# Optimization experiments

Measured on AMD Instinct MI355X. Metric: run time of the kernel, lower is better.

Reference implementation:

```python
import jax, jax.numpy as jnp
import numpy as np

D_MODEL = 1024
N_HEAD = 16
B, S = 4, 1024


def _linear(x, W, b):
    # torch nn.Linear: y = x @ W.T + b, W: [out, in]
    return jnp.einsum('bsd,ed->bse', x, W) + b


def _split(x):
    b, s, d = x.shape
    return x.reshape(b, s, N_HEAD, d // N_HEAD).transpose(0, 2, 1, 3)  # [b,h,s,dh]


def _concat(x):
    b, h, s, dh = x.shape
    return x.transpose(0, 2, 1, 3).reshape(b, s, h * dh)


def _attention(q, k, v):
    dh = q.shape[-1]
    scale = 1.0 / np.float32(np.sqrt(dh))
    scores = jnp.einsum('bhqd,bhkd->bhqk', q, k) * scale
    probs = jax.nn.softmax(scores, axis=-1)
    return jnp.einsum('bhqk,bhkd->bhqd', probs, v)


def setup_inputs() -> dict:
    key = jax.random.key(0)
    ks = jax.random.split(key, 20)
    sc = 1.0 / np.float32(np.sqrt(D_MODEL))
    inp = {
        'q': jax.random.normal(ks[0], (B, S, D_MODEL), jnp.float32),
        'k': jax.random.normal(ks[1], (B, S, D_MODEL), jnp.float32),
        'v': jax.random.normal(ks[2], (B, S, D_MODEL), jnp.float32),
    }
    names = ['Wq', 'Wk', 'Wv', 'Wq2', 'Wk2', 'Wv2', 'Wc', 'Wc2']
    for i, n in enumerate(names):
        inp[n] = jax.random.normal(ks[3 + i], (D_MODEL, D_MODEL), jnp.float32) * sc
        inp['b' + n[1:]] = jnp.zeros((D_MODEL,), jnp.float32)
    return inp


def reference(q, k, v, Wq, bq, Wk, bk, Wv, bv, Wq2, bq2, Wk2, bk2, Wv2, bv2, Wc, bc, Wc2, bc2):
    # path 1 projections
    q1 = _linear(q, Wq, bq)
    k1 = _linear(k, Wk, bk)
    v1 = _linear(v, Wv, bv)
    # path 2 projections (note cross-wiring: q2 from k, k2/v2 from q)
    q2 = _linear(k, Wq2, bq2)
    k2 = _linear(q, Wk2, bk2)
    v2 = _linear(q, Wv2, bv2)

    out1 = _attention(_split(q1), _split(k1), _split(v1))
    out2 = _attention(_split(q2), _split(k2), _split(v2))

    out1 = _linear(_concat(out1), Wc, bc)
    out2 = _linear(_concat(out2), Wc2, bc2)
    return out1, out2
```

## Files before the change

### kernel.cpp

```cpp
#include <hip/hip_runtime.h>
#include <hip/hip_bf16.h>

#define B_ 4
#define S_ 1024
#define D_ 1024
#define H_ 16
#define M_ 4096

typedef unsigned short u16;
typedef __attribute__((ext_vector_type(4))) float f32x4;
typedef __attribute__((ext_vector_type(16))) float f32x16;
typedef __attribute__((ext_vector_type(8))) short short8;
typedef __attribute__((ext_vector_type(4))) u16 u16x4;

__device__ inline u16 f2bf(float f) {
  return __builtin_bit_cast(u16, __float2bfloat16(f));
}

__device__ inline short8 ldfrag(const u16* p) {
  return *reinterpret_cast<const short8*>(p);
}

__device__ inline void gload_lds16(const void* g, void* l) {
  __builtin_amdgcn_global_load_lds((const __attribute__((address_space(1))) void*)g,
                                   (__attribute__((address_space(3))) void*)l,
                                   16, 0, 0);
}

__device__ inline int sigma_s(int s) {
  return (s & ~12) | ((s & 4) << 1) | ((s & 8) >> 1);
}

struct GArgs {
  const void* A[6];
  const void* W[6];
  const float* bias[6];
  void* C[6];
  float oscale[6];
  int vtrans[6];
};

struct CvtArgs {
  const float* src[11];
  u16* dst[11];
  int n4[11];
};

__global__ __launch_bounds__(256) void cvt_f32_bf16(CvtArgs a) {
  const int z = blockIdx.y;
  const float4* s = (const float4*)a.src[z];
  u16x4* d = (u16x4*)a.dst[z];
  const int n4 = a.n4[z];
  for (int i = blockIdx.x * blockDim.x + threadIdx.x; i < n4; i += gridDim.x * blockDim.x) {
    float4 v = s[i];
    u16x4 o;
    o[0] = f2bf(v.x); o[1] = f2bf(v.y); o[2] = f2bf(v.z); o[3] = f2bf(v.w);
    d[i] = o;
  }
}

template<typename CT>
__global__ __launch_bounds__(512, 1) void gemm_ring(GArgs args) {
  const int z = blockIdx.z;
  const u16* A = (const u16*)args.A[z];
  const u16* W = (const u16*)args.W[z];
  const float* bias = args.bias[z];
  CT* C = (CT*)args.C[z];
  const float oscale = args.oscale[z];
  const int vtrans = args.vtrans[z];

  __shared__ u16 LA[3][256 * 64];
  __shared__ u16 LB[3][128 * 64];

  const int tid = threadIdx.x;
  const int lane = tid & 63;
  const int w = tid >> 6;
  const int wm = w >> 1, wn = w & 1;
  const int l15 = lane & 15, lhi = lane >> 4;

  const int nwg = gridDim.x * gridDim.y;
  const int lin = blockIdx.x + blockIdx.y * gridDim.x;
  const int swz = (lin & 7) * (nwg >> 3) + (lin >> 3);
  const int bx = swz % gridDim.x, by = swz / gridDim.x;
  const int m0 = by * 256, n0 = bx * 128;

  const int srow = tid >> 3;
  const int sgcol = (((tid & 7) ^ (srow & 7)) << 3);

  f32x4 acc[4][4];
#pragma unroll
  for (int m = 0; m < 4; ++m)
#pragma unroll
    for (int n = 0; n < 4; ++n) acc[m][n] = f32x4{0.f, 0.f, 0.f, 0.f};

  const u16* Abase = A + (size_t)m0 * 1024;
  const u16* Wbase = W + (size_t)n0 * 1024;

  auto stage = [&](int ktile, int r) {
    const u16* Ag = Abase + ktile * 64;
    const u16* Wg = Wbase + ktile * 64;
#pragma unroll
    for (int i = 0; i < 4; ++i)
      gload_lds16(Ag + (size_t)(i * 64 + srow) * 1024 + sgcol, &LA[r][i * 4096 + w * 512]);
#pragma unroll
    for (int i = 0; i < 2; ++i)
      gload_lds16(Wg + (size_t)(i * 64 + srow) * 1024 + sgcol, &LB[r][i * 4096 + w * 512]);
  };

  stage(0, 0);
  stage(1, 1);
  asm volatile("s_waitcnt vmcnt(6)" ::: "memory");
  __builtin_amdgcn_s_barrier();
  __builtin_amdgcn_sched_barrier(0);

  for (int t = 0; t < 16; ++t) {
    const int kp = (t + 2 < 16) ? t + 2 : 15;
    stage(kp, (t + 2) % 3);

    const int r = t % 3;
#pragma unroll
    for (int kk = 0; kk < 2; ++kk) {
      short8 af[4], bf[4];
#pragma unroll
      for (int m = 0; m < 4; ++m) {
        int row = wm * 64 + m * 16 + l15;
        af[m] = ldfrag(&LA[r][row * 64 + (((kk * 4 + lhi) ^ (row & 7)) << 3)]);
      }
#pragma unroll
      for (int n = 0; n < 4; ++n) {
        int row = wn * 64 + n * 16 + l15;
        bf[n] = ldfrag(&LB[r][row * 64 + (((kk * 4 + lhi) ^ (row & 7)) << 3)]);
      }
      __builtin_amdgcn_s_setprio(1);
#pragma unroll
      for (int m = 0; m < 4; ++m)
#pragma unroll
        for (int n = 0; n < 4; ++n)
          acc[m][n] = __builtin_amdgcn_mfma_f32_16x16x32_bf16(af[m], bf[n], acc[m][n], 0, 0, 0);
      __builtin_amdgcn_s_setprio(0);
    }

    asm volatile("s_waitcnt vmcnt(6)" ::: "memory");
    __builtin_amdgcn_s_barrier();
    __builtin_amdgcn_sched_barrier(0);
  }

#pragma unroll
  for (int m = 0; m < 4; ++m) {
#pragma unroll
    for (int n = 0; n < 4; ++n) {
      int ncol = n0 + wn * 64 + n * 16 + l15;
      float bsv = bias[ncol];
      int mb = m0 + wm * 64 + m * 16 + lhi * 4;
      if (vtrans) {
        int h = ncol >> 6, d = ncol & 63;
        int b = mb >> 10, s0 = sigma_s(mb & 1023);
        u16x4 ov;
#pragma unroll
        for (int r2 = 0; r2 < 4; ++r2) ov[r2] = f2bf((acc[m][n][r2] + bsv) * oscale);
        *reinterpret_cast<u16x4*>((u16*)C + ((size_t)((b * 16 + h) * 64 + d)) * 1024 + s0) = ov;
      } else {
#pragma unroll
        for (int r2 = 0; r2 < 4; ++r2) {
          float val = (acc[m][n][r2] + bsv) * oscale;
          if constexpr (sizeof(CT) == 2) ((u16*)C)[(size_t)(mb + r2) * 1024 + ncol] = f2bf(val);
          else ((float*)C)[(size_t)(mb + r2) * 1024 + ncol] = val;
        }
      }
    }
  }
}

template<typename AT, typename CT>
__global__ __launch_bounds__(256) void gemm_bt_batched(GArgs args) {
  const int z = blockIdx.z;
  const AT* A = (const AT*)args.A[z];
  const float* W = (const float*)args.W[z];
  const float* bias = args.bias[z];
  CT* C = (CT*)args.C[z];
  const float oscale = args.oscale[z];
  const int vtrans = args.vtrans[z];

  __shared__ u16 Al[128][72];
  __shared__ u16 Bl[128][72];

  const int tid = threadIdx.x;
  const int lane = tid & 63;
  const int wid = tid >> 6;
  const int wr = wid >> 1, wc = wid & 1;
  const int m0 = blockIdx.y * 128, n0 = blockIdx.x * 128;
  const int l15 = lane & 15, lhi = lane >> 4;

  const f32x4 vzero = {0.f, 0.f, 0.f, 0.f};
  f32x4 acc[4][4];
#pragma unroll
  for (int i = 0; i < 4; ++i)
#pragma unroll
    for (int j = 0; j < 4; ++j) acc[i][j] = vzero;

  for (int kt = 0; kt < 1024; kt += 64) {
    __syncthreads();
#pragma unroll
    for (int i = 0; i < 8; ++i) {
      int g = tid + i * 256;
      int row = g >> 4, col = (g & 15) * 4;
      u16x4 bv;
      if constexpr (sizeof(AT) == 4) {
        float4 vv = *reinterpret_cast<const float4*>((const float*)A + (size_t)(m0 + row) * 1024 + kt + col);
        bv[0] = f2bf(vv.x); bv[1] = f2bf(vv.y); bv[2] = f2bf(vv.z); bv[3] = f2bf(vv.w);
      } else {
        bv = *reinterpret_cast<const u16x4*>((const u16*)A + (size_t)(m0 + row) * 1024 + kt + col);
      }
      *reinterpret_cast<u16x4*>(&Al[row][col]) = bv;
    }
#pragma unroll
    for (int i = 0; i < 8; ++i) {
      int g = tid + i * 256;
      int row = g >> 4, col = (g & 15) * 4;
      float4 vv = *reinterpret_cast<const float4*>((const float*)W + (size_t)(n0 + row) * 1024 + kt + col);
      u16x4 bv;
      bv[0] = f2bf(vv.x); bv[1] = f2bf(vv.y); bv[2] = f2bf(vv.z); bv[3] = f2bf(vv.w);
      *reinterpret_cast<u16x4*>(&Bl[row][col]) = bv;
    }
    __syncthreads();

#pragma unroll
    for (int c = 0; c < 2; ++c) {
      short8 af[4], bfr[4];
#pragma unroll
      for (int i = 0; i < 4; ++i) af[i] = ldfrag(&Al[wr * 64 + i * 16 + l15][c * 32 + lhi * 8]);
#pragma unroll
      for (int j = 0; j < 4; ++j) bfr[j] = ldfrag(&Bl[wc * 64 + j * 16 + l15][c * 32 + lhi * 8]);
#pragma unroll
      for (int i = 0; i < 4; ++i)
#pragma unroll
        for (int j = 0; j < 4; ++j)
          acc[i][j] = __builtin_amdgcn_mfma_f32_16x16x32_bf16(af[i], bfr[j], acc[i][j], 0, 0, 0);
    }
  }

#pragma unroll
  for (int i = 0; i < 4; ++i) {
#pragma unroll
    for (int j = 0; j < 4; ++j) {
      int n = n0 + wc * 64 + j * 16 + l15;
      float bsv = bias[n];
      int mb = m0 + wr * 64 + i * 16 + lhi * 4;
      if (vtrans) {
        int h = n >> 6, d = n & 63;
        int b = mb >> 10, s0 = sigma_s(mb & 1023);
        u16x4 ov;
#pragma unroll
        for (int r = 0; r < 4; ++r) ov[r] = f2bf((acc[i][j][r] + bsv) * oscale);
        *reinterpret_cast<u16x4*>((u16*)C + ((size_t)((b * 16 + h) * 64 + d)) * 1024 + s0) = ov;
      } else {
#pragma unroll
        for (int r = 0; r < 4; ++r) {
          float val = (acc[i][j][r] + bsv) * oscale;
          if constexpr (sizeof(CT) == 2) ((u16*)C)[(size_t)(mb + r) * 1024 + n] = f2bf(val);
          else ((float*)C)[(size_t)(mb + r) * 1024 + n] = val;
        }
      }
    }
  }
}

__global__ __launch_bounds__(256, 2) void attn_fused32b(const u16* q1b, const u16* k1b, const u16* vt1,
                                                        const u16* q2b, const u16* k2b, const u16* vt2,
                                                        u16* o1, u16* o2) {
  const int qt = blockIdx.x;
  const int h = blockIdx.y;
  const int zb = blockIdx.z;
  const int path = zb >> 2, b = zb & 3;

  const u16* Q = (path == 0) ? q1b : q2b;
  const u16* K = (path == 0) ? k1b : k2b;
  const u16* V = (path == 0) ? vt1 : vt2;
  u16* O = (path == 0) ? o1 : o2;

  const size_t base_qk = (size_t)b * S_ * D_ + (size_t)h * 64;
  const size_t vbase = (size_t)((b * 16 + h) * 64) * 1024;
  const int tid = threadIdx.x;
  const int lane = tid & 63, w = tid >> 6;
  const int lq = lane & 31, hi = lane >> 5;

  __shared__ u16 Ks[2][64][72];
  __shared__ u16 Vs[2][64][72];

  const int srow = tid >> 3;
  const int scol = (tid & 7) * 8;

  const int qbase_row = qt * 256 + w * 64;
  short8 qf[2][4];
#pragma unroll
  for (int qtile = 0; qtile < 2; ++qtile)
#pragma unroll
    for (int dhg = 0; dhg < 4; ++dhg)
      qf[qtile][dhg] = ldfrag(Q + base_qk + (size_t)(qbase_row + qtile * 32 + lq) * 1024 + dhg * 16 + hi * 8);

  f32x16 o_acc[2][2] = {};
  float m_r[2] = {-1e30f, -1e30f};
  float l_r[2] = {0.f, 0.f};

  {
    short8 r0 = ldfrag(K + base_qk + (size_t)srow * 1024 + scol);
    short8 r1 = ldfrag(K + base_qk + (size_t)(srow + 32) * 1024 + scol);
    short8 r2 = ldfrag(V + vbase + (size_t)srow * 1024 + scol);
    short8 r3 = ldfrag(V + vbase + (size_t)(srow + 32) * 1024 + scol);
    *reinterpret_cast<short8*>(&Ks[0][srow][scol]) = r0;
    *reinterpret_cast<short8*>(&Ks[0][srow + 32][scol]) = r1;
    *reinterpret_cast<short8*>(&Vs[0][srow][scol]) = r2;
    *reinterpret_cast<short8*>(&Vs[0][srow + 32][scol]) = r3;
  }
  __syncthreads();

  for (int kv = 0; kv < 16; ++kv) {
    const int cur = kv & 1;

    short8 n0, n1, n2, n3;
    if (kv < 15) {
      const u16* kg = K + base_qk + (size_t)((kv + 1) * 64) * 1024;
      const u16* vg = V + vbase + (kv + 1) * 64;
      n0 = ldfrag(kg + (size_t)srow * 1024 + scol);
      n1 = ldfrag(kg + (size_t)(srow + 32) * 1024 + scol);
      n2 = ldfrag(vg + (size_t)srow * 1024 + scol);
      n3 = ldfrag(vg + (size_t)(srow + 32) * 1024 + scol);
    }

    f32x16 s[2][2] = {};
    __builtin_amdgcn_s_setprio(1);
#pragma unroll
    for (int dhg = 0; dhg < 4; ++dhg) {
#pragma unroll
      for (int keytile = 0; keytile < 2; ++keytile) {
        short8 ka = ldfrag(&Ks[cur][keytile * 32 + lq][dhg * 16 + hi * 8]);
#pragma unroll
        for (int qtile = 0; qtile < 2; ++qtile)
          s[keytile][qtile] = __builtin_amdgcn_mfma_f32_32x32x16_bf16(ka, qf[qtile][dhg], s[keytile][qtile], 0, 0, 0);
      }
    }
    __builtin_amdgcn_s_setprio(0);

#pragma unroll
    for (int qtile = 0; qtile < 2; ++qtile) {
      float pm = s[0][qtile][0];
#pragma unroll
      for (int r = 1; r < 16; ++r) pm = fmaxf(pm, s[0][qtile][r]);
#pragma unroll
      for (int r = 0; r < 16; ++r) pm = fmaxf(pm, s[1][qtile][r]);
      pm = fmaxf(pm, __shfl_xor(pm, 32));
      float mn = fmaxf(m_r[qtile], pm);
      float sc = __expf(m_r[qtile] - mn);
      m_r[qtile] = mn;
      float sum = 0.f;
#pragma unroll
      for (int kt = 0; kt < 2; ++kt)
#pragma unroll
        for (int r = 0; r < 16; ++r) {
          float e = __expf(s[kt][qtile][r] - mn);
          s[kt][qtile][r] = e;
          sum += e;
        }
      sum += __shfl_xor(sum, 32);
      l_r[qtile] = l_r[qtile] * sc + sum;
      o_acc[0][qtile] *= sc;
      o_acc[1][qtile] *= sc;
    }

    __builtin_amdgcn_s_setprio(1);
#pragma unroll
    for (int g = 0; g < 4; ++g) {
      short8 va0 = ldfrag(&Vs[cur][lq][g * 16 + hi * 8]);
      short8 va1 = ldfrag(&Vs[cur][32 + lq][g * 16 + hi * 8]);
#pragma unroll
      for (int qtile = 0; qtile < 2; ++qtile) {
        short8 pb;
#pragma unroll
        for (int j = 0; j < 8; ++j) {
          float pv = (g < 2) ? s[0][qtile][(g & 1) * 8 + j] : s[1][qtile][(g & 1) * 8 + j];
          pb[j] = (short)f2bf(pv);
        }
        o_acc[0][qtile] = __builtin_amdgcn_mfma_f32_32x32x16_bf16(va0, pb, o_acc[0][qtile], 0, 0, 0);
        o_acc[1][qtile] = __builtin_amdgcn_mfma_f32_32x32x16_bf16(va1, pb, o_acc[1][qtile], 0, 0, 0);
      }
    }
    __builtin_amdgcn_s_setprio(0);

    __syncthreads();
    if (kv < 15) {
      const int nxt = cur ^ 1;
      *reinterpret_cast<short8*>(&Ks[nxt][srow][scol]) = n0;
      *reinterpret_cast<short8*>(&Ks[nxt][srow + 32][scol]) = n1;
      *reinterpret_cast<short8*>(&Vs[nxt][srow][scol]) = n2;
      *reinterpret_cast<short8*>(&Vs[nxt][srow + 32][scol]) = n3;
      __syncthreads();
    }
  }

#pragma unroll
  for (int qtile = 0; qtile < 2; ++qtile) {
    float inv = 1.0f / l_r[qtile];
    u16* Op = O + base_qk + (size_t)(qbase_row + qtile * 32 + lq) * 1024;
#pragma unroll
    for (int dtile = 0; dtile < 2; ++dtile) {
#pragma unroll
      for (int qd = 0; qd < 4; ++qd) {
        u16x4 ov;
#pragma unroll
        for (int r = 0; r < 4; ++r) ov[r] = f2bf(o_acc[dtile][qtile][qd * 4 + r] * inv);
        *reinterpret_cast<u16x4*>(Op + dtile * 32 + 8 * qd + 4 * hi) = ov;
      }
    }
  }
}

extern "C" void kernel_launch(void* const* d_in, const int* in_sizes, int n_in,
                              void* d_out, int out_size, void* d_ws, size_t ws_size,
                              hipStream_t stream) {
  const float* q   = (const float*)d_in[0];
  const float* k   = (const float*)d_in[1];
  const float* v   = (const float*)d_in[2];
  const float* Wq  = (const float*)d_in[3];  const float* bq  = (const float*)d_in[4];
  const float* Wk  = (const float*)d_in[5];  const float* bk  = (const float*)d_in[6];
  const float* Wv  = (const float*)d_in[7];  const float* bv  = (const float*)d_in[8];
  const float* Wq2 = (const float*)d_in[9];  const float* bq2 = (const float*)d_in[10];
  const float* Wk2 = (const float*)d_in[11]; const float* bk2 = (const float*)d_in[12];
  const float* Wv2 = (const float*)d_in[13]; const float* bv2 = (const float*)d_in[14];
  const float* Wc  = (const float*)d_in[15]; const float* bc  = (const float*)d_in[16];
  const float* Wc2 = (const float*)d_in[17]; const float* bc2 = (const float*)d_in[18];

  u16* ws = (u16*)d_ws;
  const size_t SZ = (size_t)M_ * D_;
  const size_t WSZ = (size_t)D_ * D_;
  u16* q1b = ws + 0 * SZ;
  u16* k1b = ws + 1 * SZ;
  u16* vt1 = ws + 2 * SZ;
  u16* q2b = ws + 3 * SZ;
  u16* k2b = ws + 4 * SZ;
  u16* vt2 = ws + 5 * SZ;
  u16* a1  = ws + 6 * SZ;
  u16* a2  = ws + 7 * SZ;

  const size_t need = (11 * SZ + 8 * WSZ) * sizeof(u16);

  if (ws_size >= need) {
    u16* qb = ws + 8 * SZ;
    u16* kb = ws + 9 * SZ;
    u16* vb = ws + 10 * SZ;
    u16* wbase = ws + 11 * SZ;
    u16* WqB  = wbase + 0 * WSZ;
    u16* WkB  = wbase + 1 * WSZ;
    u16* WvB  = wbase + 2 * WSZ;
    u16* Wq2B = wbase + 3 * WSZ;
    u16* Wk2B = wbase + 4 * WSZ;
    u16* Wv2B = wbase + 5 * WSZ;
    u16* WcB  = wbase + 6 * WSZ;
    u16* Wc2B = wbase + 7 * WSZ;

    CvtArgs ca;
    ca.src[0] = q;   ca.dst[0] = qb;   ca.n4[0] = (int)(SZ / 4);
    ca.src[1] = k;   ca.dst[1] = kb;   ca.n4[1] = (int)(SZ / 4);
    ca.src[2] = v;   ca.dst[2] = vb;   ca.n4[2] = (int)(SZ / 4);
    ca.src[3] = Wq;  ca.dst[3] = WqB;  ca.n4[3] = (int)(WSZ / 4);
    ca.src[4] = Wk;  ca.dst[4] = WkB;  ca.n4[4] = (int)(WSZ / 4);
    ca.src[5] = Wv;  ca.dst[5] = WvB;  ca.n4[5] = (int)(WSZ / 4);
    ca.src[6] = Wq2; ca.dst[6] = Wq2B; ca.n4[6] = (int)(WSZ / 4);
    ca.src[7] = Wk2; ca.dst[7] = Wk2B; ca.n4[7] = (int)(WSZ / 4);
    ca.src[8] = Wv2; ca.dst[8] = Wv2B; ca.n4[8] = (int)(WSZ / 4);
    ca.src[9] = Wc;  ca.dst[9] = WcB;  ca.n4[9] = (int)(WSZ / 4);
    ca.src[10] = Wc2; ca.dst[10] = Wc2B; ca.n4[10] = (int)(WSZ / 4);
    cvt_f32_bf16<<<dim3(512, 11), dim3(256), 0, stream>>>(ca);

    GArgs pa;
    pa.A[0] = qb; pa.W[0] = WqB;  pa.bias[0] = bq;  pa.C[0] = q1b; pa.oscale[0] = 0.125f; pa.vtrans[0] = 0;
    pa.A[1] = kb; pa.W[1] = WkB;  pa.bias[1] = bk;  pa.C[1] = k1b; pa.oscale[1] = 1.0f;   pa.vtrans[1] = 0;
    pa.A[2] = vb; pa.W[2] = WvB;  pa.bias[2] = bv;  pa.C[2] = vt1; pa.oscale[2] = 1.0f;   pa.vtrans[2] = 1;
    pa.A[3] = kb; pa.W[3] = Wq2B; pa.bias[3] = bq2; pa.C[3] = q2b; pa.oscale[3] = 0.125f; pa.vtrans[3] = 0;
    pa.A[4] = qb; pa.W[4] = Wk2B; pa.bias[4] = bk2; pa.C[4] = k2b; pa.oscale[4] = 1.0f;   pa.vtrans[4] = 0;
    pa.A[5] = qb; pa.W[5] = Wv2B; pa.bias[5] = bv2; pa.C[5] = vt2; pa.oscale[5] = 1.0f;   pa.vtrans[5] = 1;
    gemm_ring<u16><<<dim3(8, 16, 6), dim3(512), 0, stream>>>(pa);

    attn_fused32b<<<dim3(4, 16, 8), dim3(256), 0, stream>>>(q1b, k1b, vt1, q2b, k2b, vt2, a1, a2);

    GArgs fa;
    fa.A[0] = a1; fa.W[0] = WcB;  fa.bias[0] = bc;  fa.C[0] = (float*)d_out;      fa.oscale[0] = 1.0f; fa.vtrans[0] = 0;
    fa.A[1] = a2; fa.W[1] = Wc2B; fa.bias[1] = bc2; fa.C[1] = (float*)d_out + SZ; fa.oscale[1] = 1.0f; fa.vtrans[1] = 0;
    gemm_ring<float><<<dim3(8, 16, 2), dim3(512), 0, stream>>>(fa);
  } else {
    GArgs pa;
    pa.A[0] = q; pa.W[0] = Wq;  pa.bias[0] = bq;  pa.C[0] = q1b; pa.oscale[0] = 0.125f; pa.vtrans[0] = 0;
    pa.A[1] = k; pa.W[1] = Wk;  pa.bias[1] = bk;  pa.C[1] = k1b; pa.oscale[1] = 1.0f;   pa.vtrans[1] = 0;
    pa.A[2] = v; pa.W[2] = Wv;  pa.bias[2] = bv;  pa.C[2] = vt1; pa.oscale[2] = 1.0f;   pa.vtrans[2] = 1;
    pa.A[3] = k; pa.W[3] = Wq2; pa.bias[3] = bq2; pa.C[3] = q2b; pa.oscale[3] = 0.125f; pa.vtrans[3] = 0;
    pa.A[4] = q; pa.W[4] = Wk2; pa.bias[4] = bk2; pa.C[4] = k2b; pa.oscale[4] = 1.0f;   pa.vtrans[4] = 0;
    pa.A[5] = q; pa.W[5] = Wv2; pa.bias[5] = bv2; pa.C[5] = vt2; pa.oscale[5] = 1.0f;   pa.vtrans[5] = 1;
    gemm_bt_batched<float, u16><<<dim3(8, 32, 6), dim3(256), 0, stream>>>(pa);

    attn_fused32b<<<dim3(4, 16, 8), dim3(256), 0, stream>>>(q1b, k1b, vt1, q2b, k2b, vt2, a1, a2);

    GArgs fa;
    fa.A[0] = a1; fa.W[0] = Wc;  fa.bias[0] = bc;  fa.C[0] = (float*)d_out;      fa.oscale[0] = 1.0f; fa.vtrans[0] = 0;
    fa.A[1] = a2; fa.W[1] = Wc2; fa.bias[1] = bc2; fa.C[1] = (float*)d_out + SZ; fa.oscale[1] = 1.0f; fa.vtrans[1] = 0;
    gemm_bt_batched<u16, float><<<dim3(8, 32, 2), dim3(256), 0, stream>>>(fa);
  }
}
```

Baseline: 180.4 us.

## Split projection GEMM K-step into two phases interleaving global loads with MFMA

```diff
diff --git a/kernel.cpp b/kernel.cpp
--- a/kernel.cpp
+++ b/kernel.cpp
@@ -96,49 +96,84 @@
   const u16* Abase = A + (size_t)m0 * 1024;
   const u16* Wbase = W + (size_t)n0 * 1024;
 
-  auto stage = [&](int ktile, int r) {
-    const u16* Ag = Abase + ktile * 64;
-    const u16* Wg = Wbase + ktile * 64;
-#pragma unroll
-    for (int i = 0; i < 4; ++i)
-      gload_lds16(Ag + (size_t)(i * 64 + srow) * 1024 + sgcol, &LA[r][i * 4096 + w * 512]);
-#pragma unroll
-    for (int i = 0; i < 2; ++i)
-      gload_lds16(Wg + (size_t)(i * 64 + srow) * 1024 + sgcol, &LB[r][i * 4096 + w * 512]);
+  auto stageA = [&](int ktile, int r, int i) {
+    gload_lds16(Abase + ktile * 64 + (size_t)(i * 64 + srow) * 1024 + sgcol,
+                &LA[r][i * 4096 + w * 512]);
   };
-
-  stage(0, 0);
-  stage(1, 1);
+  auto stageB = [&](int ktile, int r, int i) {
+    gload_lds16(Wbase + ktile * 64 + (size_t)(i * 64 + srow) * 1024 + sgcol,
+                &LB[r][i * 4096 + w * 512]);
+  };
+
+#pragma unroll
+  for (int i = 0; i < 4; ++i) stageA(0, 0, i);
+  stageB(0, 0, 0); stageB(0, 0, 1);
+#pragma unroll
+  for (int i = 0; i < 4; ++i) stageA(1, 1, i);
+  stageB(1, 1, 0); stageB(1, 1, 1);
   asm volatile("s_waitcnt vmcnt(6)" ::: "memory");
   __builtin_amdgcn_s_barrier();
   __builtin_amdgcn_sched_barrier(0);
 
   for (int t = 0; t < 16; ++t) {
     const int kp = (t + 2 < 16) ? t + 2 : 15;
-    stage(kp, (t + 2) % 3);
-
+    const int rn = (t + 2) % 3;
     const int r = t % 3;
+
+    stageA(kp, rn, 0);
+    stageA(kp, rn, 1);
+    stageA(kp, rn, 2);
+
+    short8 bf[2][4], af0[2][2];
 #pragma unroll
     for (int kk = 0; kk < 2; ++kk) {
-      short8 af[4], bf[4];
-#pragma unroll
-      for (int m = 0; m < 4; ++m) {
-        int row = wm * 64 + m * 16 + l15;
-        af[m] = ldfrag(&LA[r][row * 64 + (((kk * 4 + lhi) ^ (row & 7)) << 3)]);
-      }
 #pragma unroll
       for (int n = 0; n < 4; ++n) {
         int row = wn * 64 + n * 16 + l15;
-        bf[n] = ldfrag(&LB[r][row * 64 + (((kk * 4 + lhi) ^ (row & 7)) << 3)]);
-      }
-      __builtin_amdgcn_s_setprio(1);
-#pragma unroll
-      for (int m = 0; m < 4; ++m)
+        bf[kk][n] = ldfrag(&LB[r][row * 64 + (((kk * 4 + lhi) ^ (row & 7)) << 3)]);
+      }
+#pragma unroll
+      for (int m = 0; m < 2; ++m) {
+        int row = wm * 64 + m * 16 + l15;
+        af0[kk][m] = ldfrag(&LA[r][row * 64 + (((kk * 4 + lhi) ^ (row & 7)) << 3)]);
+      }
+    }
+    asm volatile("s_waitcnt lgkmcnt(0)" ::: "memory");
+    __builtin_amdgcn_sched_barrier(0);
+    __builtin_amdgcn_s_setprio(1);
+#pragma unroll
+    for (int kk = 0; kk < 2; ++kk)
+#pragma unroll
+      for (int m = 0; m < 2; ++m)
 #pragma unroll
         for (int n = 0; n < 4; ++n)
-          acc[m][n] = __builtin_amdgcn_mfma_f32_16x16x32_bf16(af[m], bf[n], acc[m][n], 0, 0, 0);
-      __builtin_amdgcn_s_setprio(0);
-    }
+          acc[m][n] = __builtin_amdgcn_mfma_f32_16x16x32_bf16(af0[kk][m], bf[kk][n], acc[m][n], 0, 0, 0);
+    __builtin_amdgcn_s_setprio(0);
+    __builtin_amdgcn_s_barrier();
+
+    stageA(kp, rn, 3);
+    stageB(kp, rn, 0);
+    stageB(kp, rn, 1);
+
+    short8 af1[2][2];
+#pragma unroll
+    for (int kk = 0; kk < 2; ++kk)
+#pragma unroll
+      for (int m = 0; m < 2; ++m) {
+        int row = wm * 64 + (m + 2) * 16 + l15;
+        af1[kk][m] = ldfrag(&LA[r][row * 64 + (((kk * 4 + lhi) ^ (row & 7)) << 3)]);
+      }
+    asm volatile("s_waitcnt lgkmcnt(0)" ::: "memory");
+    __builtin_amdgcn_sched_barrier(0);
+    __builtin_amdgcn_s_setprio(1);
+#pragma unroll
+    for (int kk = 0; kk < 2; ++kk)
+#pragma unroll
+      for (int m = 0; m < 2; ++m)
+#pragma unroll
+        for (int n = 0; n < 4; ++n)
+          acc[m + 2][n] = __builtin_amdgcn_mfma_f32_16x16x32_bf16(af1[kk][m], bf[kk][n], acc[m + 2][n], 0, 0, 0);
+    __builtin_amdgcn_s_setprio(0);
 
     asm volatile("s_waitcnt vmcnt(6)" ::: "memory");
     __builtin_amdgcn_s_barrier();
```

After: 197.0 us. +9.2%, slower.
